# Kernel tuning notes

Hardware: AMD Instinct MI355X
Metric: run time of the kernel (lower is better)

The kernel has to match this reference:

```python
import jax, jax.numpy as jnp
import numpy as np

EMBED = 768
HEAD = 64
SEQ = 4096
BATCH = 4


def setup_inputs() -> dict:
    key = jax.random.key(0)
    ks = jax.random.split(key, 7)
    s = 1.0 / np.sqrt(EMBED)
    x = jax.random.normal(ks[0], (BATCH, SEQ, EMBED), dtype=jnp.float32)
    Wq = jax.random.uniform(ks[1], (EMBED, HEAD), jnp.float32, -s, s)
    bq = jax.random.uniform(ks[2], (HEAD,), jnp.float32, -s, s)
    Wk = jax.random.uniform(ks[3], (EMBED, HEAD), jnp.float32, -s, s)
    bk = jax.random.uniform(ks[4], (HEAD,), jnp.float32, -s, s)
    Wv = jax.random.uniform(ks[5], (EMBED, HEAD), jnp.float32, -s, s)
    bv = jax.random.uniform(ks[6], (HEAD,), jnp.float32, -s, s)
    return {"x": x, "Wq": Wq, "bq": bq, "Wk": Wk, "bk": bk, "Wv": Wv, "bv": bv}


def reference(x, Wq, bq, Wk, bk, Wv, bv):
    # x: [B,T,E]
    Q = x @ Wq + bq  # [B,T,H]
    K = x @ Wk + bk
    V = x @ Wv + bv
    scale = 1.0 / jnp.sqrt(jnp.asarray(HEAD, dtype=x.dtype))
    wei = jnp.einsum('bqh,bkh->bqk', Q, K) * scale  # [B,T,T]
    T = x.shape[1]
    causal = jnp.tril(jnp.ones((T, T), dtype=bool))
    wei = jnp.where(causal, wei, -jnp.inf)
    wei = jax.nn.softmax(wei, axis=-1)
    return jnp.einsum('bqk,bkh->bqh', wei, V)  # [B,T,H]
```

## Files before the change

kernel.cpp:

```cpp
#include <hip/hip_runtime.h>


#define BB 4
#define TT 4096
#define EE 768
#define HH 64
#define BT (BB*TT)

typedef __attribute__((ext_vector_type(8))) short short8;
typedef __attribute__((ext_vector_type(4))) float f32x4;
#define MFMA16(a,b,c) __builtin_amdgcn_mfma_f32_16x16x32_bf16(a,b,c,0,0,0)
#define QSCALE 0.18033688011112042f

static __device__ __forceinline__ float bflo(unsigned a){ return __uint_as_float(a << 16); }
static __device__ __forceinline__ unsigned short f2bf(float f){
    unsigned x = __float_as_uint(f);
    x += 0x7fffu + ((x >> 16) & 1u);
    return (unsigned short)(x >> 16);
}
template<int FP32>
static __device__ __forceinline__ float ldin(const void* p, int idx){
    if (FP32) return ((const float*)p)[idx];
    return bflo(((const unsigned short*)p)[idx]);
}

template<int FP32>
static __device__ void wt_body(const void* W, int wi, int e0, unsigned short* wt){
    __shared__ unsigned short ts[64 * 72];
    const int tid = threadIdx.x;
    #pragma unroll
    for (int p = 0; p < 2; p++){
        int i = p * 256 + tid;
        int r = i >> 3, g = i & 7;
        unsigned short v[8];
        if (FP32){
            const float* src = (const float*)W + (size_t)(e0 + r) * HH + g * 8;
            const float4 a = *(const float4*)src, b = *(const float4*)(src + 4);
            v[0]=f2bf(a.x); v[1]=f2bf(a.y); v[2]=f2bf(a.z); v[3]=f2bf(a.w);
            v[4]=f2bf(b.x); v[5]=f2bf(b.y); v[6]=f2bf(b.z); v[7]=f2bf(b.w);
        } else {
            const unsigned short* src = (const unsigned short*)W + (size_t)(e0 + r) * HH + g * 8;
            #pragma unroll
            for (int j = 0; j < 8; j++) v[j] = src[j];
        }
        #pragma unroll
        for (int j = 0; j < 8; j++) ts[r * 72 + g * 8 + j] = v[j];
    }
    __syncthreads();
    #pragma unroll
    for (int p = 0; p < 2; p++){
        int i = p * 256 + tid;
        int h = i >> 3, g = i & 7;
        unsigned short v[8];
        #pragma unroll
        for (int j = 0; j < 8; j++) v[j] = ts[(g * 8 + j) * 72 + h];
        unsigned short* dst = wt + (size_t)(wi * 64 + h) * EE + e0 + g * 8;
        uint4 pk;
        pk.x = (unsigned)v[0] | ((unsigned)v[1] << 16);
        pk.y = (unsigned)v[2] | ((unsigned)v[3] << 16);
        pk.z = (unsigned)v[4] | ((unsigned)v[5] << 16);
        pk.w = (unsigned)v[6] | ((unsigned)v[7] << 16);
        *(uint4*)dst = pk;
    }
}
__global__ __launch_bounds__(256) void wt_kernel(
    const unsigned short* xu, const void* Wq, const void* Wk, const void* Wv,
    unsigned short* wt, int* flag){
    __shared__ int cnt;
    const int tid = threadIdx.x;
    if (tid == 0) cnt = 0;
    __syncthreads();
    int c = 0;
    #pragma unroll
    for (int i = 0; i < 16; i++){
        unsigned u = xu[tid * 16 + i];
        unsigned e = (u >> 7) & 0xFFu;
        if (e >= 140u) c++;
    }
    atomicAdd(&cnt, c);
    __syncthreads();
    const int fp32 = (cnt > 32) ? 1 : 0;
    if (blockIdx.x == 0 && tid == 0) *flag = fp32;
    const int wi = blockIdx.x / 12;
    const int e0 = (blockIdx.x % 12) * 64;
    const void* W = (wi == 0) ? Wq : (wi == 1) ? Wk : Wv;
    if (fp32) wt_body<1>(W, wi, e0, wt);
    else      wt_body<0>(W, wi, e0, wt);
}

template<int FP32>
static __device__ void qkv_body(const void* x, const unsigned short* wt,
    const void* bq, const void* bk, const void* bv,
    unsigned short* Qw, unsigned short* Kw, unsigned short* VTw,
    unsigned short* xs, unsigned short* wsl)
{
    const int tid = threadIdx.x, lane = tid & 63, w = tid >> 6;
    const int l15 = lane & 15, quad = lane >> 4;
    const int z = blockIdx.x;
    const int m0 = (z >> 1) * 32;
    const int nh = z & 1;
    const int rh = (w & 1) * 16;
    const int ngl = (w >> 1) * 3;

    f32x4 acc[3];
    #pragma unroll
    for (int i = 0; i < 3; i++) acc[i] = (f32x4)(0.f);

    const int srow = tid >> 3, sg = tid & 7;

    for (int c = 0; c < 12; c++){
        const int c0 = c * 64;
        __syncthreads();
        {
            short8 v;
            if (FP32){
                const float* src = (const float*)x + (size_t)(m0 + srow) * EE + c0 + sg * 8;
                const float4 a = *(const float4*)src, b2 = *(const float4*)(src + 4);
                v[0]=(short)f2bf(a.x); v[1]=(short)f2bf(a.y); v[2]=(short)f2bf(a.z); v[3]=(short)f2bf(a.w);
                v[4]=(short)f2bf(b2.x); v[5]=(short)f2bf(b2.y); v[6]=(short)f2bf(b2.z); v[7]=(short)f2bf(b2.w);
            } else {
                v = *(const short8*)((const unsigned short*)x + (size_t)(m0 + srow) * EE + c0 + sg * 8);
            }
            *(short8*)&xs[srow * 72 + sg * 8] = v;
        }
        #pragma unroll
        for (int p = 0; p < 3; p++){
            int i = p * 256 + tid;
            int n = i >> 3, g2 = i & 7;
            *(short8*)&wsl[n * 72 + g2 * 8] =
                *(const short8*)(wt + (size_t)(nh * 96 + n) * EE + c0 + g2 * 8);
        }
        __syncthreads();
        #pragma unroll
        for (int kst = 0; kst < 2; kst++){
            const short8 a = *(const short8*)&xs[(rh + l15) * 72 + kst * 32 + quad * 8];
            #pragma unroll
            for (int nf = 0; nf < 3; nf++){
                const short8 bfr = *(const short8*)&wsl[((ngl + nf) * 16 + l15) * 72 + kst * 32 + quad * 8];
                acc[nf] = MFMA16(a, bfr, acc[nf]);
            }
        }
    }
    #pragma unroll
    for (int nf = 0; nf < 3; nf++){
        const int gi = nh * 6 + ngl + nf;
        const int wi = gi >> 2;
        const int h = (gi & 3) * 16 + l15;
        const void* bp = (wi == 0) ? bq : (wi == 1) ? bk : bv;
        const float bias = ldin<FP32>(bp, h);
        if (wi == 0){
            #pragma unroll
            for (int rr = 0; rr < 4; rr++){
                const int tok = m0 + rh + quad * 4 + rr;
                Qw[(size_t)tok * HH + h] = f2bf((acc[nf][rr] + bias) * QSCALE);
            }
        } else if (wi == 1){
            #pragma unroll
            for (int rr = 0; rr < 4; rr++){
                const int tok = m0 + rh + quad * 4 + rr;
                Kw[(size_t)tok * HH + h] = f2bf(acc[nf][rr] + bias);
            }
        } else {
            const int tok0 = m0 + rh + quad * 4;
            const int bloc = tok0 >> 12;
            const int tl = tok0 & 4095;
            uint2 pk;
            pk.x = (unsigned)f2bf(acc[nf][0] + bias) | ((unsigned)f2bf(acc[nf][1] + bias) << 16);
            pk.y = (unsigned)f2bf(acc[nf][2] + bias) | ((unsigned)f2bf(acc[nf][3] + bias) << 16);
            *(uint2*)&VTw[(size_t)(bloc * 64 + h) * TT + tl] = pk;
        }
    }
}
__global__ __launch_bounds__(256, 4) void qkv_kernel(
    const void* x, const unsigned short* wt,
    const void* bq, const void* bk, const void* bv,
    unsigned short* Qw, unsigned short* Kw, unsigned short* VTw, const int* flag){
    __shared__ unsigned short xs[32 * 72];
    __shared__ unsigned short wsl[96 * 72];
    if (*flag) qkv_body<1>(x, wt, bq, bk, bv, Qw, Kw, VTw, xs, wsl);
    else       qkv_body<0>(x, wt, bq, bk, bv, Qw, Kw, VTw, xs, wsl);
}

__global__ __launch_bounds__(512, 2) void attn_kernel(
    const unsigned short* __restrict__ Q,
    const unsigned short* __restrict__ K, const unsigned short* __restrict__ VT,
    void* __restrict__ out, const int* __restrict__ flag)
{
    __shared__ unsigned short sbuf[8][2304];
    __shared__ float lpart[8][32];

    const int mode = *flag;
    const int z = blockIdx.x;
    const int b = z & 3;
    const int qt = 127 - (z >> 2);
    const int q0 = qt * 32;
    const int nkb = (qt >> 1) + 1;
    const int tid = threadIdx.x;
    const int lane = tid & 63;
    const int w = tid >> 6;
    const int l15 = lane & 15, quad = lane >> 4;
    const int brow = b * TT;

    f32x4 O[2][4];
    float lsum[2][4];
    #pragma unroll
    for (int mt = 0; mt < 2; mt++)
        #pragma unroll
        for (int i = 0; i < 4; i++){ O[mt][i] = (f32x4)(0.f); lsum[mt][i] = 0.f; }

    if (w < nkb){
        short8 qf[2][2];
        #pragma unroll
        for (int mt = 0; mt < 2; mt++)
            #pragma unroll
            for (int kst = 0; kst < 2; kst++)
                qf[mt][kst] = *(const short8*)(Q + (size_t)(brow + q0 + mt * 16 + l15) * HH + kst * 32 + quad * 8);

        short8 kf[4][2];
        #pragma unroll
        for (int c = 0; c < 4; c++)
            #pragma unroll
            for (int kst = 0; kst < 2; kst++)
                kf[c][kst] = *(const short8*)(K + (size_t)(brow + w * 64 + c * 16 + l15) * HH + kst * 32 + quad * 8);

        for (int u = w; u < nkb; u += 8){
            const int k0 = u * 64;
            f32x4 sacc[2][4];
            #pragma unroll
            for (int mt = 0; mt < 2; mt++)
                #pragma unroll
                for (int c = 0; c < 4; c++){
                    sacc[mt][c] = (f32x4)(0.f);
                    sacc[mt][c] = MFMA16(qf[mt][0], kf[c][0], sacc[mt][c]);
                    sacc[mt][c] = MFMA16(qf[mt][1], kf[c][1], sacc[mt][c]);
                }
            short8 vf[4][2];
            #pragma unroll
            for (int c = 0; c < 4; c++)
                #pragma unroll
                for (int kst = 0; kst < 2; kst++)
                    vf[c][kst] = *(const short8*)(VT + (size_t)(b * 64 + c * 16 + l15) * TT + k0 + kst * 32 + quad * 8);
            if (u + 8 < nkb){
                const int kn0 = (u + 8) * 64;
                #pragma unroll
                for (int c = 0; c < 4; c++)
                    #pragma unroll
                    for (int kst = 0; kst < 2; kst++)
                        kf[c][kst] = *(const short8*)(K + (size_t)(brow + kn0 + c * 16 + l15) * HH + kst * 32 + quad * 8);
            }
            const bool diag = (u == nkb - 1);
            #pragma unroll
            for (int mt = 0; mt < 2; mt++){
                #pragma unroll
                for (int c = 0; c < 4; c++){
                    #pragma unroll
                    for (int rr = 0; rr < 4; rr++){
                        float sv = sacc[mt][c][rr];
                        if (diag){
                            const int kg = k0 + c * 16 + l15;
                            const int qg = q0 + mt * 16 + quad * 4 + rr;
                            sv = (kg <= qg) ? sv : -1e30f;
                        }
                        const float p = exp2f(sv);
                        lsum[mt][rr] += p;
                        sbuf[w][mt * 1152 + (quad * 4 + rr) * 72 + c * 16 + l15] = f2bf(p);
                    }
                }
            }
            #pragma unroll
            for (int mt = 0; mt < 2; mt++){
                const short8 pf0 = *(const short8*)&sbuf[w][mt * 1152 + l15 * 72 + quad * 8];
                const short8 pf1 = *(const short8*)&sbuf[w][mt * 1152 + l15 * 72 + 32 + quad * 8];
                #pragma unroll
                for (int c2 = 0; c2 < 4; c2++){
                    O[mt][c2] = MFMA16(pf0, vf[c2][0], O[mt][c2]);
                    O[mt][c2] = MFMA16(pf1, vf[c2][1], O[mt][c2]);
                }
            }
        }
        #pragma unroll
        for (int mt = 0; mt < 2; mt++)
            #pragma unroll
            for (int rr = 0; rr < 4; rr++){
                #pragma unroll
                for (int off = 1; off < 16; off <<= 1)
                    lsum[mt][rr] += __shfl_xor(lsum[mt][rr], off, 64);
            }
    }
    #pragma unroll
    for (int mt = 0; mt < 2; mt++)
        #pragma unroll
        for (int rr = 0; rr < 4; rr++){
            const int row = mt * 16 + quad * 4 + rr;
            #pragma unroll
            for (int c2 = 0; c2 < 4; c2++)
                sbuf[w][row * 72 + c2 * 16 + l15] = f2bf(O[mt][c2][rr]);
            if (l15 == 0) lpart[w][row] = lsum[mt][rr];
        }
    __syncthreads();
    #pragma unroll
    for (int i = 0; i < 4; i++){
        const int e = i * 512 + tid;
        const int r = e >> 6, h = e & 63;
        float num = 0.f, den = 0.f;
        #pragma unroll
        for (int ww = 0; ww < 8; ww++){
            num += bflo(sbuf[ww][r * 72 + h]);
            den += lpart[ww][r];
        }
        const float ov = num / den;
        const size_t gi = (size_t)(brow + q0 + r) * HH + h;
        if (mode) ((float*)out)[gi] = ov;
        else      ((unsigned short*)out)[gi] = f2bf(ov);
    }
}

extern "C" void kernel_launch(void* const* d_in, const int* in_sizes, int n_in,
                              void* d_out, int out_size, void* d_ws, size_t ws_size,
                              hipStream_t stream) {
    const void* x  = d_in[0];
    const void* Wq = d_in[1];
    const void* bq = d_in[2];
    const void* Wk = d_in[3];
    const void* bk = d_in[4];
    const void* Wv = d_in[5];
    const void* bv = d_in[6];

    unsigned short* Qw  = (unsigned short*)d_ws;
    unsigned short* Kw  = Qw + (size_t)BT * HH;
    unsigned short* VTw = Kw + (size_t)BT * HH;
    unsigned short* wt  = VTw + (size_t)BT * HH;
    int* flag  = (int*)(wt + (size_t)192 * EE);

    wt_kernel<<<36, 256, 0, stream>>>((const unsigned short*)x, Wq, Wk, Wv, wt, flag);
    qkv_kernel<<<1024, 256, 0, stream>>>(x, wt, bq, bk, bv, Qw, Kw, VTw, flag);
    attn_kernel<<<512, 512, 0, stream>>>(Qw, Kw, VTw, d_out, flag);
}
```

Measured before the change: 159.3 us.

## Fuse weight transpose into QKV kernel and keep P in registers via shuffles

Removes the separate weight-transpose kernel: each QKV block now detects the input dtype itself and transposes W tiles straight into shared memory, which saves a launch. In attention, S is computed transposed (K as the A operand), so the softmax probabilities are packed into bf16 pairs with a byte-permute (truncation instead of round-to-nearest). They are then redistributed across lanes with shuffles instead of a round trip through LDS, and the row-sum reduction shrinks to two shuffles. The cost is extra shuffle instructions and scattered 2-byte LDS stores during the W transpose.

```diff
diff --git a/kernel.cpp b/kernel.cpp
--- a/kernel.cpp
+++ b/kernel.cpp
@@ -9,6 +9,7 @@
 
 typedef __attribute__((ext_vector_type(8))) short short8;
 typedef __attribute__((ext_vector_type(4))) float f32x4;
+typedef __attribute__((ext_vector_type(4))) unsigned uint4v;
 #define MFMA16(a,b,c) __builtin_amdgcn_mfma_f32_16x16x32_bf16(a,b,c,0,0,0)
 #define QSCALE 0.18033688011112042f
 
@@ -18,6 +19,9 @@
     x += 0x7fffu + ((x >> 16) & 1u);
     return (unsigned short)(x >> 16);
 }
+static __device__ __forceinline__ unsigned pk2bf(float lo, float hi){
+    return __builtin_amdgcn_perm(__float_as_uint(hi), __float_as_uint(lo), 0x07060302u);
+}
 template<int FP32>
 static __device__ __forceinline__ float ldin(const void* p, int idx){
     if (FP32) return ((const float*)p)[idx];
@@ -25,71 +29,8 @@
 }
 
 template<int FP32>
-static __device__ void wt_body(const void* W, int wi, int e0, unsigned short* wt){
-    __shared__ unsigned short ts[64 * 72];
-    const int tid = threadIdx.x;
-    #pragma unroll
-    for (int p = 0; p < 2; p++){
-        int i = p * 256 + tid;
-        int r = i >> 3, g = i & 7;
-        unsigned short v[8];
-        if (FP32){
-            const float* src = (const float*)W + (size_t)(e0 + r) * HH + g * 8;
-            const float4 a = *(const float4*)src, b = *(const float4*)(src + 4);
-            v[0]=f2bf(a.x); v[1]=f2bf(a.y); v[2]=f2bf(a.z); v[3]=f2bf(a.w);
-            v[4]=f2bf(b.x); v[5]=f2bf(b.y); v[6]=f2bf(b.z); v[7]=f2bf(b.w);
-        } else {
-            const unsigned short* src = (const unsigned short*)W + (size_t)(e0 + r) * HH + g * 8;
-            #pragma unroll
-            for (int j = 0; j < 8; j++) v[j] = src[j];
-        }
-        #pragma unroll
-        for (int j = 0; j < 8; j++) ts[r * 72 + g * 8 + j] = v[j];
-    }
-    __syncthreads();
-    #pragma unroll
-    for (int p = 0; p < 2; p++){
-        int i = p * 256 + tid;
-        int h = i >> 3, g = i & 7;
-        unsigned short v[8];
-        #pragma unroll
-        for (int j = 0; j < 8; j++) v[j] = ts[(g * 8 + j) * 72 + h];
-        unsigned short* dst = wt + (size_t)(wi * 64 + h) * EE + e0 + g * 8;
-        uint4 pk;
-        pk.x = (unsigned)v[0] | ((unsigned)v[1] << 16);
-        pk.y = (unsigned)v[2] | ((unsigned)v[3] << 16);
-        pk.z = (unsigned)v[4] | ((unsigned)v[5] << 16);
-        pk.w = (unsigned)v[6] | ((unsigned)v[7] << 16);
-        *(uint4*)dst = pk;
-    }
-}
-__global__ __launch_bounds__(256) void wt_kernel(
-    const unsigned short* xu, const void* Wq, const void* Wk, const void* Wv,
-    unsigned short* wt, int* flag){
-    __shared__ int cnt;
-    const int tid = threadIdx.x;
-    if (tid == 0) cnt = 0;
-    __syncthreads();
-    int c = 0;
-    #pragma unroll
-    for (int i = 0; i < 16; i++){
-        unsigned u = xu[tid * 16 + i];
-        unsigned e = (u >> 7) & 0xFFu;
-        if (e >= 140u) c++;
-    }
-    atomicAdd(&cnt, c);
-    __syncthreads();
-    const int fp32 = (cnt > 32) ? 1 : 0;
-    if (blockIdx.x == 0 && tid == 0) *flag = fp32;
-    const int wi = blockIdx.x / 12;
-    const int e0 = (blockIdx.x % 12) * 64;
-    const void* W = (wi == 0) ? Wq : (wi == 1) ? Wk : Wv;
-    if (fp32) wt_body<1>(W, wi, e0, wt);
-    else      wt_body<0>(W, wi, e0, wt);
-}
-
-template<int FP32>
-static __device__ void qkv_body(const void* x, const unsigned short* wt,
+static __device__ void qkv_body(const void* x,
+    const void* Wq, const void* Wk, const void* Wv,
     const void* bq, const void* bk, const void* bv,
     unsigned short* Qw, unsigned short* Kw, unsigned short* VTw,
     unsigned short* xs, unsigned short* wsl)
@@ -107,6 +48,7 @@
     for (int i = 0; i < 3; i++) acc[i] = (f32x4)(0.f);
 
     const int srow = tid >> 3, sg = tid & 7;
+    const int e_l = tid & 63, ng8b = tid >> 6;
 
     for (int c = 0; c < 12; c++){
         const int c0 = c * 64;
@@ -125,10 +67,25 @@
         }
         #pragma unroll
         for (int p = 0; p < 3; p++){
-            int i = p * 256 + tid;
-            int n = i >> 3, g2 = i & 7;
-            *(short8*)&wsl[n * 72 + g2 * 8] =
-                *(const short8*)(wt + (size_t)(nh * 96 + n) * EE + c0 + g2 * 8);
+            const int ng8 = p * 4 + ng8b;
+            const int n0 = ng8 * 8;
+            const int ngg = nh * 96 + n0;
+            const int wi = ngg >> 6;
+            const int h0 = ngg & 63;
+            const void* W = (wi == 0) ? Wq : (wi == 1) ? Wk : Wv;
+            unsigned short v[8];
+            if (FP32){
+                const float* src = (const float*)W + (size_t)(c0 + e_l) * HH + h0;
+                const float4 a = *(const float4*)src, b2 = *(const float4*)(src + 4);
+                v[0]=f2bf(a.x); v[1]=f2bf(a.y); v[2]=f2bf(a.z); v[3]=f2bf(a.w);
+                v[4]=f2bf(b2.x); v[5]=f2bf(b2.y); v[6]=f2bf(b2.z); v[7]=f2bf(b2.w);
+            } else {
+                const unsigned short* src = (const unsigned short*)W + (size_t)(c0 + e_l) * HH + h0;
+                #pragma unroll
+                for (int j = 0; j < 8; j++) v[j] = src[j];
+            }
+            #pragma unroll
+            for (int j = 0; j < 8; j++) wsl[(n0 + j) * 72 + e_l] = v[j];
         }
         __syncthreads();
         #pragma unroll
@@ -164,21 +121,36 @@
             const int tok0 = m0 + rh + quad * 4;
             const int bloc = tok0 >> 12;
             const int tl = tok0 & 4095;
-            uint2 pk;
-            pk.x = (unsigned)f2bf(acc[nf][0] + bias) | ((unsigned)f2bf(acc[nf][1] + bias) << 16);
-            pk.y = (unsigned)f2bf(acc[nf][2] + bias) | ((unsigned)f2bf(acc[nf][3] + bias) << 16);
-            *(uint2*)&VTw[(size_t)(bloc * 64 + h) * TT + tl] = pk;
+            uint2 pkk;
+            pkk.x = (unsigned)f2bf(acc[nf][0] + bias) | ((unsigned)f2bf(acc[nf][1] + bias) << 16);
+            pkk.y = (unsigned)f2bf(acc[nf][2] + bias) | ((unsigned)f2bf(acc[nf][3] + bias) << 16);
+            *(uint2*)&VTw[(size_t)(bloc * 64 + h) * TT + tl] = pkk;
         }
     }
 }
 __global__ __launch_bounds__(256, 4) void qkv_kernel(
-    const void* x, const unsigned short* wt,
+    const void* x, const void* Wq, const void* Wk, const void* Wv,
     const void* bq, const void* bk, const void* bv,
-    unsigned short* Qw, unsigned short* Kw, unsigned short* VTw, const int* flag){
+    unsigned short* Qw, unsigned short* Kw, unsigned short* VTw, int* flag){
     __shared__ unsigned short xs[32 * 72];
     __shared__ unsigned short wsl[96 * 72];
-    if (*flag) qkv_body<1>(x, wt, bq, bk, bv, Qw, Kw, VTw, xs, wsl);
-    else       qkv_body<0>(x, wt, bq, bk, bv, Qw, Kw, VTw, xs, wsl);
+    __shared__ int cnt;
+    const int tid = threadIdx.x;
+    if (tid == 0) cnt = 0;
+    __syncthreads();
+    int c = 0;
+    #pragma unroll
+    for (int i = 0; i < 16; i++){
+        unsigned u = ((const unsigned short*)x)[tid * 16 + i];
+        unsigned e = (u >> 7) & 0xFFu;
+        if (e >= 140u) c++;
+    }
+    atomicAdd(&cnt, c);
+    __syncthreads();
+    const int fp32 = (cnt > 32) ? 1 : 0;
+    if (blockIdx.x == 0 && tid == 0) *flag = fp32;
+    if (fp32) qkv_body<1>(x, Wq, Wk, Wv, bq, bk, bv, Qw, Kw, VTw, xs, wsl);
+    else      qkv_body<0>(x, Wq, Wk, Wv, bq, bk, bv, Qw, Kw, VTw, xs, wsl);
 }
 
 __global__ __launch_bounds__(512, 2) void attn_kernel(
@@ -199,104 +171,116 @@
     const int lane = tid & 63;
     const int w = tid >> 6;
     const int l15 = lane & 15, quad = lane >> 4;
-    const int brow = b * TT;
 
     f32x4 O[2][4];
-    float lsum[2][4];
+    float lsum[2] = {0.f, 0.f};
     #pragma unroll
     for (int mt = 0; mt < 2; mt++)
         #pragma unroll
-        for (int i = 0; i < 4; i++){ O[mt][i] = (f32x4)(0.f); lsum[mt][i] = 0.f; }
+        for (int i = 0; i < 4; i++) O[mt][i] = (f32x4)(0.f);
 
     if (w < nkb){
+        const unsigned short* Kb  = K  + (size_t)b * TT * HH;
+        const unsigned short* VTb = VT + (size_t)b * 64 * TT;
         short8 qf[2][2];
         #pragma unroll
         for (int mt = 0; mt < 2; mt++)
             #pragma unroll
             for (int kst = 0; kst < 2; kst++)
-                qf[mt][kst] = *(const short8*)(Q + (size_t)(brow + q0 + mt * 16 + l15) * HH + kst * 32 + quad * 8);
-
+                qf[mt][kst] = *(const short8*)(Q + ((size_t)b * TT + q0 + mt * 16 + l15) * HH + kst * 32 + quad * 8);
+        int kO[4], vO[4];
+        #pragma unroll
+        for (int c = 0; c < 4; c++){
+            kO[c] = (c * 16 + l15) * HH + quad * 8;
+            vO[c] = (c * 16 + l15) * TT + quad * 8;
+        }
+        const int srcA0 = l15 + ((quad & 1) << 5);
+        const int csel = quad >> 1;
         short8 kf[4][2];
         #pragma unroll
         for (int c = 0; c < 4; c++)
             #pragma unroll
             for (int kst = 0; kst < 2; kst++)
-                kf[c][kst] = *(const short8*)(K + (size_t)(brow + w * 64 + c * 16 + l15) * HH + kst * 32 + quad * 8);
+                kf[c][kst] = *(const short8*)(Kb + w * 64 * HH + kO[c] + kst * 32);
 
         for (int u = w; u < nkb; u += 8){
             const int k0 = u * 64;
-            f32x4 sacc[2][4];
+            f32x4 st[2][4];
             #pragma unroll
             for (int mt = 0; mt < 2; mt++)
                 #pragma unroll
                 for (int c = 0; c < 4; c++){
-                    sacc[mt][c] = (f32x4)(0.f);
-                    sacc[mt][c] = MFMA16(qf[mt][0], kf[c][0], sacc[mt][c]);
-                    sacc[mt][c] = MFMA16(qf[mt][1], kf[c][1], sacc[mt][c]);
+                    st[mt][c] = (f32x4)(0.f);
+                    st[mt][c] = MFMA16(kf[c][0], qf[mt][0], st[mt][c]);
+                    st[mt][c] = MFMA16(kf[c][1], qf[mt][1], st[mt][c]);
                 }
             short8 vf[4][2];
             #pragma unroll
             for (int c = 0; c < 4; c++)
                 #pragma unroll
                 for (int kst = 0; kst < 2; kst++)
-                    vf[c][kst] = *(const short8*)(VT + (size_t)(b * 64 + c * 16 + l15) * TT + k0 + kst * 32 + quad * 8);
+                    vf[c][kst] = *(const short8*)(VTb + vO[c] + k0 + kst * 32);
             if (u + 8 < nkb){
-                const int kn0 = (u + 8) * 64;
                 #pragma unroll
                 for (int c = 0; c < 4; c++)
                     #pragma unroll
                     for (int kst = 0; kst < 2; kst++)
-                        kf[c][kst] = *(const short8*)(K + (size_t)(brow + kn0 + c * 16 + l15) * HH + kst * 32 + quad * 8);
+                        kf[c][kst] = *(const short8*)(Kb + (u + 8) * 64 * HH + kO[c] + kst * 32);
             }
             const bool diag = (u == nkb - 1);
             #pragma unroll
             for (int mt = 0; mt < 2; mt++){
+                unsigned pk[4][2];
                 #pragma unroll
                 for (int c = 0; c < 4; c++){
+                    float pe[4];
                     #pragma unroll
-                    for (int rr = 0; rr < 4; rr++){
-                        float sv = sacc[mt][c][rr];
+                    for (int rg = 0; rg < 4; rg++){
+                        float sv = st[mt][c][rg];
                         if (diag){
-                            const int kg = k0 + c * 16 + l15;
-                            const int qg = q0 + mt * 16 + quad * 4 + rr;
+                            const int kg = k0 + c * 16 + quad * 4 + rg;
+                            const int qg = q0 + mt * 16 + l15;
                             sv = (kg <= qg) ? sv : -1e30f;
                         }
-                        const float p = exp2f(sv);
-                        lsum[mt][rr] += p;
-                        sbuf[w][mt * 1152 + (quad * 4 + rr) * 72 + c * 16 + l15] = f2bf(p);
+                        pe[rg] = exp2f(sv);
+                        lsum[mt] += pe[rg];
                     }
+                    pk[c][0] = pk2bf(pe[0], pe[1]);
+                    pk[c][1] = pk2bf(pe[2], pe[3]);
                 }
-            }
-            #pragma unroll
-            for (int mt = 0; mt < 2; mt++){
-                const short8 pf0 = *(const short8*)&sbuf[w][mt * 1152 + l15 * 72 + quad * 8];
-                const short8 pf1 = *(const short8*)&sbuf[w][mt * 1152 + l15 * 72 + 32 + quad * 8];
-                #pragma unroll
-                for (int c2 = 0; c2 < 4; c2++){
-                    O[mt][c2] = MFMA16(pf0, vf[c2][0], O[mt][c2]);
-                    O[mt][c2] = MFMA16(pf1, vf[c2][1], O[mt][c2]);
+                #pragma unroll
+                for (int kst = 0; kst < 2; kst++){
+                    union { uint4v u4; short8 s; } af;
+                    #pragma unroll
+                    for (int pp = 0; pp < 4; pp++){
+                        const int src = srcA0 + ((pp >> 1) << 4);
+                        const unsigned a0 = (unsigned)__shfl((int)pk[kst * 2][pp & 1], src, 64);
+                        const unsigned a1 = (unsigned)__shfl((int)pk[kst * 2 + 1][pp & 1], src, 64);
+                        af.u4[pp] = csel ? a1 : a0;
+                    }
+                    #pragma unroll
+                    for (int c2 = 0; c2 < 4; c2++)
+                        O[mt][c2] = MFMA16(af.s, vf[c2][kst], O[mt][c2]);
                 }
             }
         }
         #pragma unroll
-        for (int mt = 0; mt < 2; mt++)
-            #pragma unroll
-            for (int rr = 0; rr < 4; rr++){
-                #pragma unroll
-                for (int off = 1; off < 16; off <<= 1)
-                    lsum[mt][rr] += __shfl_xor(lsum[mt][rr], off, 64);
-            }
-    }
-    #pragma unroll
-    for (int mt = 0; mt < 2; mt++)
+        for (int mt = 0; mt < 2; mt++){
+            lsum[mt] += __shfl_xor(lsum[mt], 16, 64);
+            lsum[mt] += __shfl_xor(lsum[mt], 32, 64);
+        }
+    }
+    #pragma unroll
+    for (int mt = 0; mt < 2; mt++){
         #pragma unroll
         for (int rr = 0; rr < 4; rr++){
             const int row = mt * 16 + quad * 4 + rr;
             #pragma unroll
             for (int c2 = 0; c2 < 4; c2++)
                 sbuf[w][row * 72 + c2 * 16 + l15] = f2bf(O[mt][c2][rr]);
-            if (l15 == 0) lpart[w][row] = lsum[mt][rr];
-        }
+        }
+        if (quad == 0) lpart[w][mt * 16 + l15] = lsum[mt];
+    }
     __syncthreads();
     #pragma unroll
     for (int i = 0; i < 4; i++){
@@ -309,7 +293,7 @@
             den += lpart[ww][r];
         }
         const float ov = num / den;
-        const size_t gi = (size_t)(brow + q0 + r) * HH + h;
+        const size_t gi = ((size_t)b * TT + q0 + r) * HH + h;
         if (mode) ((float*)out)[gi] = ov;
         else      ((unsigned short*)out)[gi] = f2bf(ov);
     }
@@ -329,10 +313,8 @@
     unsigned short* Qw  = (unsigned short*)d_ws;
     unsigned short* Kw  = Qw + (size_t)BT * HH;
     unsigned short* VTw = Kw + (size_t)BT * HH;
-    unsigned short* wt  = VTw + (size_t)BT * HH;
-    int* flag  = (int*)(wt + (size_t)192 * EE);
-
-    wt_kernel<<<36, 256, 0, stream>>>((const unsigned short*)x, Wq, Wk, Wv, wt, flag);
-    qkv_kernel<<<1024, 256, 0, stream>>>(x, wt, bq, bk, bv, Qw, Kw, VTw, flag);
+    int* flag = (int*)(VTw + (size_t)BT * HH);
+
+    qkv_kernel<<<1024, 256, 0, stream>>>(x, Wq, Wk, Wv, bq, bk, bv, Qw, Kw, VTw, flag);
     attn_kernel<<<512, 512, 0, stream>>>(Qw, Kw, VTw, d_out, flag);
 }
```

Measured after the change: 169.8 us. 6.6% more time.

## Split causal attention KV range into chunks with a separate merge kernel

Applied to the files above, without the earlier changes.

The attention kernel now gives each block at most 16 key blocks of one query tile, using 256-thread blocks and a 1280-block grid with a balanced mapping of tiles to chunks. Each block writes its partial unnormalized output (bf16) and row sums to workspace, and a new merge kernel adds the chunks and divides. This is meant to fix load imbalance from long causal rows and raise the number of blocks in flight. In exchange it adds an extra launch, partial results round-tripping through global memory, and extra bf16 rounding of the partial numerators.

```diff
diff --git a/kernel.cpp b/kernel.cpp
--- a/kernel.cpp
+++ b/kernel.cpp
@@ -181,25 +181,36 @@
     else       qkv_body<0>(x, wt, bq, bk, bv, Qw, Kw, VTw, xs, wsl);
 }
 
-__global__ __launch_bounds__(512, 2) void attn_kernel(
+__global__ __launch_bounds__(256, 2) void attn_kernel(
     const unsigned short* __restrict__ Q,
     const unsigned short* __restrict__ K, const unsigned short* __restrict__ VT,
-    void* __restrict__ out, const int* __restrict__ flag)
+    float* __restrict__ pl, unsigned short* __restrict__ PO)
 {
-    __shared__ unsigned short sbuf[8][2304];
-    __shared__ float lpart[8][32];
-
-    const int mode = *flag;
+    __shared__ unsigned short sbuf[4][2304];
+    __shared__ float lpart[4][32];
+
     const int z = blockIdx.x;
     const int b = z & 3;
-    const int qt = 127 - (z >> 2);
+    const int m = z >> 2;
+    const int a = (m >= 192) ? 3 : (m >= 96) ? 2 : (m >= 32) ? 1 : 0;
+    const int seg_base = (a == 3) ? 192 : (a == 2) ? 96 : (a == 1) ? 32 : 0;
+    const int d = m - seg_base;
+    const int den = 2 * (a + 1);
+    const int Jr = d / den;
+    const int o = d - Jr * den;
+    const int nb = a + 1;
+    const int qt = 2 * (a * 16 + Jr) + (o >= nb ? 1 : 0);
+    const int chunk = (o >= nb) ? (o - nb) : o;
+
     const int q0 = qt * 32;
-    const int nkb = (qt >> 1) + 1;
+    const int v = (qt >> 1) + 1;
+    const int begin = chunk * 16;
+    const int end = (v < begin + 16) ? v : (begin + 16);
+
     const int tid = threadIdx.x;
     const int lane = tid & 63;
     const int w = tid >> 6;
     const int l15 = lane & 15, quad = lane >> 4;
-    const int brow = b * TT;
 
     f32x4 O[2][4];
     float lsum[2][4];
@@ -208,22 +219,25 @@
         #pragma unroll
         for (int i = 0; i < 4; i++){ O[mt][i] = (f32x4)(0.f); lsum[mt][i] = 0.f; }
 
-    if (w < nkb){
+    const int u0 = begin + w;
+    if (u0 < end){
+        const unsigned short* Kb  = K  + (size_t)b * TT * HH;
+        const unsigned short* VTb = VT + (size_t)b * 64 * TT;
         short8 qf[2][2];
         #pragma unroll
         for (int mt = 0; mt < 2; mt++)
             #pragma unroll
             for (int kst = 0; kst < 2; kst++)
-                qf[mt][kst] = *(const short8*)(Q + (size_t)(brow + q0 + mt * 16 + l15) * HH + kst * 32 + quad * 8);
+                qf[mt][kst] = *(const short8*)(Q + ((size_t)b * TT + q0 + mt * 16 + l15) * HH + kst * 32 + quad * 8);
 
         short8 kf[4][2];
         #pragma unroll
         for (int c = 0; c < 4; c++)
             #pragma unroll
             for (int kst = 0; kst < 2; kst++)
-                kf[c][kst] = *(const short8*)(K + (size_t)(brow + w * 64 + c * 16 + l15) * HH + kst * 32 + quad * 8);
-
-        for (int u = w; u < nkb; u += 8){
+                kf[c][kst] = *(const short8*)(Kb + (u0 * 64 + c * 16 + l15) * HH + kst * 32 + quad * 8);
+
+        for (int u = u0; u < end; u += 4){
             const int k0 = u * 64;
             f32x4 sacc[2][4];
             #pragma unroll
@@ -239,16 +253,16 @@
             for (int c = 0; c < 4; c++)
                 #pragma unroll
                 for (int kst = 0; kst < 2; kst++)
-                    vf[c][kst] = *(const short8*)(VT + (size_t)(b * 64 + c * 16 + l15) * TT + k0 + kst * 32 + quad * 8);
-            if (u + 8 < nkb){
-                const int kn0 = (u + 8) * 64;
+                    vf[c][kst] = *(const short8*)(VTb + (size_t)(c * 16 + l15) * TT + k0 + kst * 32 + quad * 8);
+            if (u + 4 < end){
+                const int kn0 = (u + 4) * 64;
                 #pragma unroll
                 for (int c = 0; c < 4; c++)
                     #pragma unroll
                     for (int kst = 0; kst < 2; kst++)
-                        kf[c][kst] = *(const short8*)(K + (size_t)(brow + kn0 + c * 16 + l15) * HH + kst * 32 + quad * 8);
-            }
-            const bool diag = (u == nkb - 1);
+                        kf[c][kst] = *(const short8*)(Kb + (size_t)(kn0 + c * 16 + l15) * HH + kst * 32 + quad * 8);
+            }
+            const bool diag = (u == v - 1);
             #pragma unroll
             for (int mt = 0; mt < 2; mt++){
                 #pragma unroll
@@ -299,20 +313,38 @@
         }
     __syncthreads();
     #pragma unroll
-    for (int i = 0; i < 4; i++){
-        const int e = i * 512 + tid;
+    for (int i = 0; i < 8; i++){
+        const int e = i * 256 + tid;
         const int r = e >> 6, h = e & 63;
-        float num = 0.f, den = 0.f;
-        #pragma unroll
-        for (int ww = 0; ww < 8; ww++){
+        float num = 0.f, dsum = 0.f;
+        #pragma unroll
+        for (int ww = 0; ww < 4; ww++){
             num += bflo(sbuf[ww][r * 72 + h]);
-            den += lpart[ww][r];
-        }
-        const float ov = num / den;
-        const size_t gi = (size_t)(brow + q0 + r) * HH + h;
-        if (mode) ((float*)out)[gi] = ov;
-        else      ((unsigned short*)out)[gi] = f2bf(ov);
-    }
+            dsum += lpart[ww][r];
+        }
+        const size_t grow = (size_t)chunk * BT + b * TT + q0 + r;
+        PO[grow * HH + h] = f2bf(num);
+        if (h == 0) pl[grow] = dsum;
+    }
+}
+
+__global__ __launch_bounds__(256) void merge_kernel(
+    const float* __restrict__ pl, const unsigned short* __restrict__ PO,
+    void* __restrict__ out, const int* __restrict__ flag)
+{
+    const int idx = blockIdx.x * 256 + threadIdx.x;
+    const int row = idx >> 6, h = idx & 63;
+    const int qt = (row & (TT - 1)) >> 5;
+    const int v = (qt >> 1) + 1;
+    const int nb = (v + 15) >> 4;
+    float num = 0.f, den = 0.f;
+    for (int s = 0; s < nb; s++){
+        num += bflo(PO[((size_t)s * BT + row) * HH + h]);
+        den += pl[(size_t)s * BT + row];
+    }
+    const float ov = num / den;
+    if (*flag) ((float*)out)[idx] = ov;
+    else       ((unsigned short*)out)[idx] = f2bf(ov);
 }
 
 extern "C" void kernel_launch(void* const* d_in, const int* in_sizes, int n_in,
@@ -330,9 +362,12 @@
     unsigned short* Kw  = Qw + (size_t)BT * HH;
     unsigned short* VTw = Kw + (size_t)BT * HH;
     unsigned short* wt  = VTw + (size_t)BT * HH;
-    int* flag  = (int*)(wt + (size_t)192 * EE);
+    unsigned short* PO  = wt + (size_t)192 * EE;
+    float* pl  = (float*)(PO + (size_t)4 * BT * HH);
+    int* flag  = (int*)(pl + (size_t)4 * BT);
 
     wt_kernel<<<36, 256, 0, stream>>>((const unsigned short*)x, Wq, Wk, Wv, wt, flag);
     qkv_kernel<<<1024, 256, 0, stream>>>(x, wt, bq, bk, bv, Qw, Kw, VTw, flag);
-    attn_kernel<<<512, 512, 0, stream>>>(Qw, Kw, VTw, d_out, flag);
-}
+    attn_kernel<<<1280, 256, 0, stream>>>(Qw, Kw, VTw, pl, PO);
+    merge_kernel<<<BT * HH / 256, 256, 0, stream>>>(pl, PO, d_out, flag);
+}
```

New measurement: 169.5 us. +6.4%, slower.
